# Optimization experiments

Measured on AMD Instinct MI355X. Metric: run time of the kernel, lower is better.

The kernel has to match this reference:

```python
import jax, jax.numpy as jnp
import numpy as np

K = 5
PAD = (K - 1) // 2
EPS_NORM = 1e-8
MASS_BOUND = 1e-7


def _window_indices(H, W):
    # For each output location (y,x) and each offset (dy,dx) in the kxk window,
    # compute the flat index of (y+dy, x+dx) in prev space and a validity mask.
    ys, xs = jnp.meshgrid(jnp.arange(H), jnp.arange(W), indexing='ij')  # [H,W]
    offs = jnp.arange(-PAD, PAD + 1)
    dy, dx = jnp.meshgrid(offs, offs, indexing='ij')  # [k,k]
    py = ys[:, :, None, None] + dy[None, None]  # [H,W,k,k]
    px = xs[:, :, None, None] + dx[None, None]
    valid = (py >= 0) & (py < H) & (px >= 0) & (px < W)
    ploc = jnp.clip(py, 0, H - 1) * W + jnp.clip(px, 0, W - 1)
    HW, KK = H * W, K * K
    return ploc.reshape(HW, KK), valid.reshape(HW, KK)


def setup_inputs() -> dict:
    key = jax.random.key(0)
    k1, k2, k3 = jax.random.split(key, 3)
    N, D, H, W = 8, 64, 64, 64
    return {
        'cur_feat': jax.random.normal(k1, (N, D, H, W), dtype=jnp.float32),
        'prev_feat': jax.random.normal(k2, (N, D, H, W), dtype=jnp.float32),
        'prev_mem': jax.random.normal(k3, (N, D, H, W), dtype=jnp.float32),
    }


def reference(cur_feat, prev_feat, prev_mem):
    N, D, H, W = prev_mem.shape
    HW = H * W
    cur = cur_feat.reshape(N, -1, HW)   # [N,Dc,HW]
    prev = prev_feat.reshape(N, -1, HW)
    # torch.norm(x, 0) = number of nonzero entries (scalar per batch)
    nc = jnp.sum(cur != 0, axis=(1, 2)).astype(cur.dtype) + EPS_NORM   # [N]
    npv = jnp.sum(prev != 0, axis=(1, 2)).astype(prev.dtype) + EPS_NORM
    # full cost volume: [N, HW(cur loc), HW(prev loc)], negatives clamped to 0
    aff = jnp.einsum('ndp,ndq->npq', cur, prev) / (nc * npv)[:, None, None]
    aff = jnp.maximum(aff, 0.0)

    ploc, valid = _window_indices(H, W)        # [HW,KK]
    loc = jnp.arange(HW)[:, None]              # [HW,1]
    coef = aff[:, loc, ploc] * valid[None].astype(aff.dtype)  # [N,HW,KK]
    mass = jnp.sum(coef, axis=-1)              # [N,HW]
    zero_mass = jnp.abs(mass) < MASS_BOUND
    w = coef / jnp.where(zero_mass, 1.0, mass)[:, :, None]    # [N,HW,KK]

    pm = prev_mem.reshape(N, D, HW)            # [N,D,HW]
    pm_win = pm[:, :, ploc]                    # [N,D,HW,KK]
    val = jnp.einsum('npk,ndpk->ndp', w, pm_win)  # weighted aggregation
    out = jnp.where(zero_mass[:, None, :], pm, val)  # mass==0 -> passthrough
    return out.reshape(N, D, H, W)
```

## Files before the change

kernel.cpp:

```cpp
#include <hip/hip_runtime.h>

#define N_  8
#define D_  64
#define H_  64
#define W_  64
#define HW_ (H_ * W_)
#define KK  25

__global__ __launch_bounds__(256) void count_nz_kernel(
    const float4* __restrict__ cur, const float4* __restrict__ prev,
    const float4* __restrict__ pmv,
    unsigned int* __restrict__ pc, unsigned int* __restrict__ pq,
    unsigned int* __restrict__ pr)
{
    __shared__ unsigned int sc[4], sp[4], sr[4];
    const int t    = threadIdx.x;
    const int wid  = t >> 6;
    const int lane = t & 63;

    unsigned int wc = 0, wp = 0, wr = 0;
#pragma unroll
    for (int j = 0; j < 4; ++j) {
        int idx = blockIdx.x * 1024 + j * 256 + t;
        float4 a = cur[idx];
        float4 b = prev[idx];
        float4 m = pmv[idx];
        wc += (unsigned)__popcll(__ballot(a.x != 0.f));
        wc += (unsigned)__popcll(__ballot(a.y != 0.f));
        wc += (unsigned)__popcll(__ballot(a.z != 0.f));
        wc += (unsigned)__popcll(__ballot(a.w != 0.f));
        wp += (unsigned)__popcll(__ballot(b.x != 0.f));
        wp += (unsigned)__popcll(__ballot(b.y != 0.f));
        wp += (unsigned)__popcll(__ballot(b.z != 0.f));
        wp += (unsigned)__popcll(__ballot(b.w != 0.f));
        wr += (unsigned)__popcll(__ballot(m.x != 0.f));
        wr += (unsigned)__popcll(__ballot(m.y != 0.f));
        wr += (unsigned)__popcll(__ballot(m.z != 0.f));
        wr += (unsigned)__popcll(__ballot(m.w != 0.f));
    }
    if (lane == 0) { sc[wid] = wc; sp[wid] = wp; sr[wid] = wr; }
    __syncthreads();
    if (t == 0) {
        pc[blockIdx.x] = sc[0] + sc[1] + sc[2] + sc[3];
        pq[blockIdx.x] = sp[0] + sp[1] + sp[2] + sp[3];
        pr[blockIdx.x] = sr[0] + sr[1] + sr[2] + sr[3];
    }
}

__global__ __launch_bounds__(512, 1) void feature_align_kernel(
    const float* __restrict__ cur, const float* __restrict__ prev,
    const float* __restrict__ pm, float* __restrict__ out,
    const unsigned int* __restrict__ pc, const unsigned int* __restrict__ pq)
{
    __shared__ float red[4][KK][128];

    const int b    = blockIdx.x;
    const int n    = b >> 5;
    const int y0   = (b & 31) * 2;
    const int lane = threadIdx.x & 63;
    const int dg   = __builtin_amdgcn_readfirstlane(threadIdx.x >> 6);
    const int r    = lane >> 5;
    const int xq   = lane & 31;
    const int x0   = xq * 2;
    const int y    = y0 + r;
    const int pix0 = r * 64 + x0;

    int cb[3];
#pragma unroll
    for (int i = 0; i < 3; ++i)
        cb[i] = min(max(x0 - 2 + 2 * i, 0), W_ - 2);
    unsigned voff[5][3];
#pragma unroll
    for (int ky = 0; ky < 5; ++ky) {
        int qy = min(max(y + ky - 2, 0), H_ - 1);
#pragma unroll
        for (int i = 0; i < 3; ++i)
            voff[ky][i] = (unsigned)((qy * W_ + cb[i]) * 4);
    }
    const unsigned curoff = (unsigned)((y * W_ + x0) * 4);

    const size_t nbase = (size_t)n * D_ * HW_;
    const char* curb  = (const char*)(cur  + nbase + (size_t)dg * 8 * HW_);
    const char* prevb = (const char*)(prev + nbase + (size_t)dg * 8 * HW_);
    const char* pmb   = (const char*)(pm   + nbase + (size_t)dg * 8 * HW_);
    char*       outb  = (char*)(out + nbase + (size_t)dg * 8 * HW_);

    float2 pmc[8];
#pragma unroll
    for (int dd = 0; dd < 8; ++dd)
        pmc[dd] = *(const float2*)(pmb + (size_t)dd * HW_ * 4 + curoff);
    unsigned int ccnt = pc[(n << 6) + lane];
    unsigned int vcnt = pq[(n << 6) + lane];

    float acc0[KK], acc1[KK];
#pragma unroll
    for (int k = 0; k < KK; ++k) { acc0[k] = 0.f; acc1[k] = 0.f; }

#pragma unroll
    for (int dd = 0; dd < 8; ++dd) {
        const char* cch = curb  + (size_t)dd * HW_ * 4;
        const char* pch = prevb + (size_t)dd * HW_ * 4;
        float2 c = *(const float2*)(cch + curoff);
        float2 t[5][3];
#pragma unroll
        for (int ky = 0; ky < 5; ++ky)
#pragma unroll
            for (int i = 0; i < 3; ++i)
                t[ky][i] = *(const float2*)(pch + voff[ky][i]);
#pragma unroll
        for (int ky = 0; ky < 5; ++ky) {
            float v[6] = { t[ky][0].x, t[ky][0].y, t[ky][1].x,
                           t[ky][1].y, t[ky][2].x, t[ky][2].y };
#pragma unroll
            for (int kx = 0; kx < 5; ++kx) {
                acc0[ky * 5 + kx] = fmaf(c.x, v[kx],     acc0[ky * 5 + kx]);
                acc1[ky * 5 + kx] = fmaf(c.y, v[kx + 1], acc1[ky * 5 + kx]);
            }
        }
    }

    if (dg < 4) {
#pragma unroll
        for (int k = 0; k < KK; ++k)
            *(float2*)&red[dg][k][pix0] = make_float2(acc0[k], acc1[k]);
    }
    __syncthreads();
    if (dg >= 4) {
#pragma unroll
        for (int k = 0; k < KK; ++k) {
            float2 t2 = *(float2*)&red[dg - 4][k][pix0];
            t2.x += acc0[k]; t2.y += acc1[k];
            *(float2*)&red[dg - 4][k][pix0] = t2;
        }
    }
    __syncthreads();

    if (threadIdx.x < 128) {
        const int pix = threadIdx.x;
        const int rr  = pix >> 6;
        const int xx  = pix & 63;

        unsigned int cc = ccnt, vv = vcnt;
#pragma unroll
        for (int s = 32; s >= 1; s >>= 1) {
            cc += __shfl_xor(cc, s);
            vv += __shfl_xor(vv, s);
        }
        float scale = 1.0f / (((float)cc + 1e-8f) * ((float)vv + 1e-8f));

        float mass = 0.f;
        float cf[KK];
#pragma unroll
        for (int k = 0; k < KK; ++k) {
            float s = red[0][k][pix] + red[1][k][pix]
                    + red[2][k][pix] + red[3][k][pix];
            int ky = k / 5, kx = k % 5;
            int py  = y0 + rr + ky - 2;
            int pxc = xx + kx - 2;
            bool val = (py >= 0) && (py < H_) && (pxc >= 0) && (pxc < W_);
            float c = val ? fmaxf(s * scale, 0.f) : 0.f;
            cf[k] = c;
            mass += c;
        }
        bool  zero = fabsf(mass) < 1e-7f;
        float inv  = zero ? 0.f : 1.0f / mass;
#pragma unroll
        for (int k = 0; k < KK; ++k) red[0][k][pix] = cf[k] * inv;
        red[1][0][pix] = zero ? 1.f : 0.f;
    }
    __syncthreads();

    const float zf0 = red[1][0][pix0];
    const float zf1 = red[1][0][pix0 + 1];

    if (zf0 != 0.f && zf1 != 0.f) {
#pragma unroll
        for (int dd = 0; dd < 8; ++dd)
            *(float2*)(outb + (size_t)dd * HW_ * 4 + curoff) = pmc[dd];
    } else {
        float w0[KK], w1[KK];
#pragma unroll
        for (int k = 0; k < KK; ++k) {
            float2 ww = *(float2*)&red[0][k][pix0];
            w0[k] = ww.x; w1[k] = ww.y;
        }
#pragma unroll
        for (int dd = 0; dd < 8; ++dd) {
            const char* pch = pmb + (size_t)dd * HW_ * 4;
            float2 t2[5][3];
#pragma unroll
            for (int ky = 0; ky < 5; ++ky)
#pragma unroll
                for (int i = 0; i < 3; ++i)
                    t2[ky][i] = *(const float2*)(pch + voff[ky][i]);
            float v0 = 0.f, v1 = 0.f;
#pragma unroll
            for (int ky = 0; ky < 5; ++ky) {
                float v[6] = { t2[ky][0].x, t2[ky][0].y, t2[ky][1].x,
                               t2[ky][1].y, t2[ky][2].x, t2[ky][2].y };
#pragma unroll
                for (int kx = 0; kx < 5; ++kx) {
                    v0 = fmaf(w0[ky * 5 + kx], v[kx],     v0);
                    v1 = fmaf(w1[ky * 5 + kx], v[kx + 1], v1);
                }
            }
            float2 o;
            o.x = (zf0 != 0.f) ? pmc[dd].x : v0;
            o.y = (zf1 != 0.f) ? pmc[dd].y : v1;
            *(float2*)(outb + (size_t)dd * HW_ * 4 + curoff) = o;
        }
    }
}

extern "C" void kernel_launch(void* const* d_in, const int* in_sizes, int n_in,
                              void* d_out, int out_size, void* d_ws, size_t ws_size,
                              hipStream_t stream)
{
    const float* cur  = (const float*)d_in[0];
    const float* prev = (const float*)d_in[1];
    const float* pm   = (const float*)d_in[2];
    float*       out  = (float*)d_out;
    unsigned int* pc  = (unsigned int*)d_ws;
    unsigned int* pq  = pc + 512;
    unsigned int* pr  = pq + 512;

    count_nz_kernel<<<512, 256, 0, stream>>>(
        (const float4*)cur, (const float4*)prev, (const float4*)pm, pc, pq, pr);

    feature_align_kernel<<<256, 512, 0, stream>>>(cur, prev, pm, out, pc, pq);
}
```

Measured before the change: 86.49 us.

## Split channels across half-waves and process one row per block

Each block now handles a single output row instead of two, doubling the grid to 512 blocks. Within a wave, the two half-waves each take four of the eight channels in the group, and their partial window sums are combined with a cross-lane shuffle before the shared-memory reduction. The launch bound is raised to allow up to four blocks per CU, and the per-thread register arrays shrink to match. The aim is to fill more of the GPU and get more latency hiding, at the cost of an extra shuffle reduction and more redundant halo loads per block.

```diff
diff --git a/kernel.cpp b/kernel.cpp
--- a/kernel.cpp
+++ b/kernel.cpp
@@ -47,24 +47,23 @@
     }
 }
 
-__global__ __launch_bounds__(512, 1) void feature_align_kernel(
+__global__ __launch_bounds__(512, 4) void feature_align_kernel(
     const float* __restrict__ cur, const float* __restrict__ prev,
     const float* __restrict__ pm, float* __restrict__ out,
     const unsigned int* __restrict__ pc, const unsigned int* __restrict__ pq)
 {
-    __shared__ float red[4][KK][128];
+    __shared__ float red[4][KK][64];
 
     const int b    = blockIdx.x;
-    const int n    = b >> 5;
-    const int y0   = (b & 31) * 2;
+    const int n    = b >> 6;
+    const int y    = b & 63;
     const int lane = threadIdx.x & 63;
     const int dg   = __builtin_amdgcn_readfirstlane(threadIdx.x >> 6);
-    const int r    = lane >> 5;
+    const int s    = lane >> 5;
     const int xq   = lane & 31;
     const int x0   = xq * 2;
-    const int y    = y0 + r;
-    const int pix0 = r * 64 + x0;
-
+
+    const unsigned laneoff = (unsigned)s * 4u * HW_ * 4u;
     int cb[3];
 #pragma unroll
     for (int i = 0; i < 3; ++i)
@@ -75,9 +74,9 @@
         int qy = min(max(y + ky - 2, 0), H_ - 1);
 #pragma unroll
         for (int i = 0; i < 3; ++i)
-            voff[ky][i] = (unsigned)((qy * W_ + cb[i]) * 4);
-    }
-    const unsigned curoff = (unsigned)((y * W_ + x0) * 4);
+            voff[ky][i] = laneoff + (unsigned)((qy * W_ + cb[i]) * 4);
+    }
+    const unsigned curoff = laneoff + (unsigned)((y * W_ + x0) * 4);
 
     const size_t nbase = (size_t)n * D_ * HW_;
     const char* curb  = (const char*)(cur  + nbase + (size_t)dg * 8 * HW_);
@@ -85,19 +84,22 @@
     const char* pmb   = (const char*)(pm   + nbase + (size_t)dg * 8 * HW_);
     char*       outb  = (char*)(out + nbase + (size_t)dg * 8 * HW_);
 
-    float2 pmc[8];
-#pragma unroll
-    for (int dd = 0; dd < 8; ++dd)
+    float2 pmc[4];
+#pragma unroll
+    for (int dd = 0; dd < 4; ++dd)
         pmc[dd] = *(const float2*)(pmb + (size_t)dd * HW_ * 4 + curoff);
-    unsigned int ccnt = pc[(n << 6) + lane];
-    unsigned int vcnt = pq[(n << 6) + lane];
+    unsigned int ccnt = 0, vcnt = 0;
+    if (dg == 0) {
+        ccnt = pc[(n << 6) + lane];
+        vcnt = pq[(n << 6) + lane];
+    }
 
     float acc0[KK], acc1[KK];
 #pragma unroll
     for (int k = 0; k < KK; ++k) { acc0[k] = 0.f; acc1[k] = 0.f; }
 
 #pragma unroll
-    for (int dd = 0; dd < 8; ++dd) {
+    for (int dd = 0; dd < 4; ++dd) {
         const char* cch = curb  + (size_t)dd * HW_ * 4;
         const char* pch = prevb + (size_t)dd * HW_ * 4;
         float2 c = *(const float2*)(cch + curoff);
@@ -119,32 +121,37 @@
         }
     }
 
+#pragma unroll
+    for (int k = 0; k < KK; ++k) {
+        acc0[k] += __shfl_xor(acc0[k], 32);
+        acc1[k] += __shfl_xor(acc1[k], 32);
+    }
+
     if (dg < 4) {
-#pragma unroll
-        for (int k = 0; k < KK; ++k)
-            *(float2*)&red[dg][k][pix0] = make_float2(acc0[k], acc1[k]);
+        if (s == 0)
+#pragma unroll
+            for (int k = 0; k < KK; ++k)
+                *(float2*)&red[dg][k][x0] = make_float2(acc0[k], acc1[k]);
     }
     __syncthreads();
     if (dg >= 4) {
-#pragma unroll
-        for (int k = 0; k < KK; ++k) {
-            float2 t2 = *(float2*)&red[dg - 4][k][pix0];
-            t2.x += acc0[k]; t2.y += acc1[k];
-            *(float2*)&red[dg - 4][k][pix0] = t2;
-        }
-    }
-    __syncthreads();
-
-    if (threadIdx.x < 128) {
-        const int pix = threadIdx.x;
-        const int rr  = pix >> 6;
-        const int xx  = pix & 63;
-
+        if (s == 0)
+#pragma unroll
+            for (int k = 0; k < KK; ++k) {
+                float2 t2 = *(float2*)&red[dg - 4][k][x0];
+                t2.x += acc0[k]; t2.y += acc1[k];
+                *(float2*)&red[dg - 4][k][x0] = t2;
+            }
+    }
+    __syncthreads();
+
+    if (dg == 0) {
+        const int pix = lane;
         unsigned int cc = ccnt, vv = vcnt;
 #pragma unroll
-        for (int s = 32; s >= 1; s >>= 1) {
-            cc += __shfl_xor(cc, s);
-            vv += __shfl_xor(vv, s);
+        for (int st = 32; st >= 1; st >>= 1) {
+            cc += __shfl_xor(cc, st);
+            vv += __shfl_xor(vv, st);
         }
         float scale = 1.0f / (((float)cc + 1e-8f) * ((float)vv + 1e-8f));
 
@@ -152,13 +159,13 @@
         float cf[KK];
 #pragma unroll
         for (int k = 0; k < KK; ++k) {
-            float s = red[0][k][pix] + red[1][k][pix]
-                    + red[2][k][pix] + red[3][k][pix];
+            float sm = red[0][k][pix] + red[1][k][pix]
+                     + red[2][k][pix] + red[3][k][pix];
             int ky = k / 5, kx = k % 5;
-            int py  = y0 + rr + ky - 2;
-            int pxc = xx + kx - 2;
+            int py  = y + ky - 2;
+            int pxc = pix + kx - 2;
             bool val = (py >= 0) && (py < H_) && (pxc >= 0) && (pxc < W_);
-            float c = val ? fmaxf(s * scale, 0.f) : 0.f;
+            float c = val ? fmaxf(sm * scale, 0.f) : 0.f;
             cf[k] = c;
             mass += c;
         }
@@ -170,22 +177,22 @@
     }
     __syncthreads();
 
-    const float zf0 = red[1][0][pix0];
-    const float zf1 = red[1][0][pix0 + 1];
+    const float zf0 = red[1][0][x0];
+    const float zf1 = red[1][0][x0 + 1];
 
     if (zf0 != 0.f && zf1 != 0.f) {
 #pragma unroll
-        for (int dd = 0; dd < 8; ++dd)
+        for (int dd = 0; dd < 4; ++dd)
             *(float2*)(outb + (size_t)dd * HW_ * 4 + curoff) = pmc[dd];
     } else {
         float w0[KK], w1[KK];
 #pragma unroll
         for (int k = 0; k < KK; ++k) {
-            float2 ww = *(float2*)&red[0][k][pix0];
+            float2 ww = *(float2*)&red[0][k][x0];
             w0[k] = ww.x; w1[k] = ww.y;
         }
 #pragma unroll
-        for (int dd = 0; dd < 8; ++dd) {
+        for (int dd = 0; dd < 4; ++dd) {
             const char* pch = pmb + (size_t)dd * HW_ * 4;
             float2 t2[5][3];
 #pragma unroll
@@ -227,5 +234,5 @@
     count_nz_kernel<<<512, 256, 0, stream>>>(
         (const float4*)cur, (const float4*)prev, (const float4*)pm, pc, pq, pr);
 
-    feature_align_kernel<<<256, 512, 0, stream>>>(cur, prev, pm, out, pc, pq);
+    feature_align_kernel<<<512, 512, 0, stream>>>(cur, prev, pm, out, pc, pq);
 }
```

After: 94.00 us. 8.7% more time.

## Fuse nonzero counting into main kernel with a grid-wide atomic barrier

Applied to the files above, without the earlier changes.

Removes the separate count kernel. Each block now counts nonzeros of cur and prev for its own tile while it loads them for the affinity computation. Blocks publish their partial counts, then meet at a spin-wait grid barrier on an atomic counter before normalizing. This drops a launch and a full extra read pass over three input tensors. In exchange it relies on all 256 blocks being co-resident, and it adds a memset and a spin barrier.

```diff
diff --git a/kernel.cpp b/kernel.cpp
--- a/kernel.cpp
+++ b/kernel.cpp
@@ -1,64 +1,28 @@
 #include <hip/hip_runtime.h>
 
-#define N_  8
-#define D_  64
-#define H_  64
-#define W_  64
-#define HW_ (H_ * W_)
-#define KK  25
-
-__global__ __launch_bounds__(256) void count_nz_kernel(
-    const float4* __restrict__ cur, const float4* __restrict__ prev,
-    const float4* __restrict__ pmv,
-    unsigned int* __restrict__ pc, unsigned int* __restrict__ pq,
-    unsigned int* __restrict__ pr)
-{
-    __shared__ unsigned int sc[4], sp[4], sr[4];
-    const int t    = threadIdx.x;
-    const int wid  = t >> 6;
-    const int lane = t & 63;
-
-    unsigned int wc = 0, wp = 0, wr = 0;
-#pragma unroll
-    for (int j = 0; j < 4; ++j) {
-        int idx = blockIdx.x * 1024 + j * 256 + t;
-        float4 a = cur[idx];
-        float4 b = prev[idx];
-        float4 m = pmv[idx];
-        wc += (unsigned)__popcll(__ballot(a.x != 0.f));
-        wc += (unsigned)__popcll(__ballot(a.y != 0.f));
-        wc += (unsigned)__popcll(__ballot(a.z != 0.f));
-        wc += (unsigned)__popcll(__ballot(a.w != 0.f));
-        wp += (unsigned)__popcll(__ballot(b.x != 0.f));
-        wp += (unsigned)__popcll(__ballot(b.y != 0.f));
-        wp += (unsigned)__popcll(__ballot(b.z != 0.f));
-        wp += (unsigned)__popcll(__ballot(b.w != 0.f));
-        wr += (unsigned)__popcll(__ballot(m.x != 0.f));
-        wr += (unsigned)__popcll(__ballot(m.y != 0.f));
-        wr += (unsigned)__popcll(__ballot(m.z != 0.f));
-        wr += (unsigned)__popcll(__ballot(m.w != 0.f));
-    }
-    if (lane == 0) { sc[wid] = wc; sp[wid] = wp; sr[wid] = wr; }
-    __syncthreads();
-    if (t == 0) {
-        pc[blockIdx.x] = sc[0] + sc[1] + sc[2] + sc[3];
-        pq[blockIdx.x] = sp[0] + sp[1] + sp[2] + sp[3];
-        pr[blockIdx.x] = sr[0] + sr[1] + sr[2] + sr[3];
-    }
-}
-
-__global__ __launch_bounds__(512, 1) void feature_align_kernel(
+#define N_   8
+#define D_   64
+#define H_   64
+#define W_   64
+#define HW_  (H_ * W_)
+#define KK   25
+#define NBLK 256
+
+__global__ __launch_bounds__(512, 1) void feature_align_fused(
     const float* __restrict__ cur, const float* __restrict__ prev,
     const float* __restrict__ pm, float* __restrict__ out,
-    const unsigned int* __restrict__ pc, const unsigned int* __restrict__ pq)
+    unsigned int* __restrict__ pc, unsigned int* __restrict__ pq,
+    unsigned int* __restrict__ bar)
 {
     __shared__ float red[4][KK][128];
+    __shared__ unsigned int swc[8];
 
     const int b    = blockIdx.x;
     const int n    = b >> 5;
     const int y0   = (b & 31) * 2;
-    const int lane = threadIdx.x & 63;
-    const int dg   = __builtin_amdgcn_readfirstlane(threadIdx.x >> 6);
+    const int tid  = threadIdx.x;
+    const int lane = tid & 63;
+    const int dg   = __builtin_amdgcn_readfirstlane(tid >> 6);
     const int r    = lane >> 5;
     const int xq   = lane & 31;
     const int x0   = xq * 2;
@@ -89,13 +53,12 @@
 #pragma unroll
     for (int dd = 0; dd < 8; ++dd)
         pmc[dd] = *(const float2*)(pmb + (size_t)dd * HW_ * 4 + curoff);
-    unsigned int ccnt = pc[(n << 6) + lane];
-    unsigned int vcnt = pq[(n << 6) + lane];
 
     float acc0[KK], acc1[KK];
 #pragma unroll
     for (int k = 0; k < KK; ++k) { acc0[k] = 0.f; acc1[k] = 0.f; }
 
+    unsigned int wc = 0, wp = 0;
 #pragma unroll
     for (int dd = 0; dd < 8; ++dd) {
         const char* cch = curb  + (size_t)dd * HW_ * 4;
@@ -107,6 +70,8 @@
 #pragma unroll
             for (int i = 0; i < 3; ++i)
                 t[ky][i] = *(const float2*)(pch + voff[ky][i]);
+        wc += (c.x != 0.f) + (c.y != 0.f);
+        wp += (t[2][1].x != 0.f) + (t[2][1].y != 0.f);
 #pragma unroll
         for (int ky = 0; ky < 5; ++ky) {
             float v[6] = { t[ky][0].x, t[ky][0].y, t[ky][1].x,
@@ -119,6 +84,12 @@
         }
     }
 
+    unsigned int pk = wc | (wp << 16);
+#pragma unroll
+    for (int st = 32; st >= 1; st >>= 1)
+        pk += __shfl_xor(pk, st);
+    if (lane == 0) swc[dg] = pk;
+
     if (dg < 4) {
 #pragma unroll
         for (int k = 0; k < KK; ++k)
@@ -133,18 +104,40 @@
             *(float2*)&red[dg - 4][k][pix0] = t2;
         }
     }
+
+    if (tid == 0) {
+        unsigned int s = 0;
+#pragma unroll
+        for (int w = 0; w < 8; ++w) s += swc[w];
+        __hip_atomic_store(&pc[b], s & 0xFFFFu, __ATOMIC_RELAXED,
+                           __HIP_MEMORY_SCOPE_AGENT);
+        __hip_atomic_store(&pq[b], s >> 16, __ATOMIC_RELAXED,
+                           __HIP_MEMORY_SCOPE_AGENT);
+        __hip_atomic_fetch_add(bar, 1u, __ATOMIC_RELEASE,
+                               __HIP_MEMORY_SCOPE_AGENT);
+        while (__hip_atomic_load(bar, __ATOMIC_ACQUIRE,
+                                 __HIP_MEMORY_SCOPE_AGENT) < NBLK)
+            __builtin_amdgcn_s_sleep(2);
+    }
     __syncthreads();
 
-    if (threadIdx.x < 128) {
-        const int pix = threadIdx.x;
+    if (tid < 128) {
+        const int pix = tid;
         const int rr  = pix >> 6;
         const int xx  = pix & 63;
-
-        unsigned int cc = ccnt, vv = vcnt;
-#pragma unroll
-        for (int s = 32; s >= 1; s >>= 1) {
-            cc += __shfl_xor(cc, s);
-            vv += __shfl_xor(vv, s);
+        const int l64 = tid & 63;
+
+        unsigned int cc = 0, vv = 0;
+        if (l64 < 32) {
+            cc = __hip_atomic_load(&pc[(n << 5) + l64], __ATOMIC_RELAXED,
+                                   __HIP_MEMORY_SCOPE_AGENT);
+            vv = __hip_atomic_load(&pq[(n << 5) + l64], __ATOMIC_RELAXED,
+                                   __HIP_MEMORY_SCOPE_AGENT);
+        }
+#pragma unroll
+        for (int st = 32; st >= 1; st >>= 1) {
+            cc += __shfl_xor(cc, st);
+            vv += __shfl_xor(vv, st);
         }
         float scale = 1.0f / (((float)cc + 1e-8f) * ((float)vv + 1e-8f));
 
@@ -152,13 +145,13 @@
         float cf[KK];
 #pragma unroll
         for (int k = 0; k < KK; ++k) {
-            float s = red[0][k][pix] + red[1][k][pix]
-                    + red[2][k][pix] + red[3][k][pix];
+            float sm = red[0][k][pix] + red[1][k][pix]
+                     + red[2][k][pix] + red[3][k][pix];
             int ky = k / 5, kx = k % 5;
             int py  = y0 + rr + ky - 2;
             int pxc = xx + kx - 2;
             bool val = (py >= 0) && (py < H_) && (pxc >= 0) && (pxc < W_);
-            float c = val ? fmaxf(s * scale, 0.f) : 0.f;
+            float c = val ? fmaxf(sm * scale, 0.f) : 0.f;
             cf[k] = c;
             mass += c;
         }
@@ -221,11 +214,10 @@
     const float* pm   = (const float*)d_in[2];
     float*       out  = (float*)d_out;
     unsigned int* pc  = (unsigned int*)d_ws;
-    unsigned int* pq  = pc + 512;
-    unsigned int* pr  = pq + 512;
-
-    count_nz_kernel<<<512, 256, 0, stream>>>(
-        (const float4*)cur, (const float4*)prev, (const float4*)pm, pc, pq, pr);
-
-    feature_align_kernel<<<256, 512, 0, stream>>>(cur, prev, pm, out, pc, pq);
+    unsigned int* pq  = pc + NBLK;
+    unsigned int* bar = pq + NBLK;
+
+    hipMemsetAsync(bar, 0, sizeof(unsigned int), stream);
+
+    feature_align_fused<<<NBLK, 512, 0, stream>>>(cur, prev, pm, out, pc, pq, bar);
 }
```

Measured after the change: 133.1 us. +53.9%, slower.
